# Kernel tuning notes

Hardware: AMD Instinct MI355X
Metric: run time of the kernel (lower is better)

## Reference

```python
import jax, jax.numpy as jnp
import numpy as np

EPS = 1e-8  # torch CosineSimilarity default eps


def setup_inputs() -> dict:
    key = jax.random.key(0)
    k1, k2, k3, k4, k5, k6, k7, k8 = jax.random.split(key, 8)
    N1, N2 = 8192, 8192
    # first 3 cols: geometric features; col 3: integer class label stored as float
    e1_feat = jax.random.normal(k1, (N1, 3), dtype=jnp.float32)
    e2_feat = jax.random.normal(k2, (N2, 3), dtype=jnp.float32)
    e1_cls = jax.random.randint(k3, (N1, 1), 0, 8).astype(jnp.float32)
    e2_cls = jax.random.randint(k4, (N2, 1), 0, 8).astype(jnp.float32)
    edges1 = jnp.concatenate([e1_feat, e1_cls], axis=-1)
    edges2 = jnp.concatenate([e2_feat, e2_cls], axis=-1)
    W1 = jax.random.normal(k5, (3, 64), dtype=jnp.float32) * 0.5
    b1 = jax.random.normal(k6, (64,), dtype=jnp.float32) * 0.1
    W2 = jax.random.normal(k7, (64, 32), dtype=jnp.float32) * 0.1
    b2 = jax.random.normal(k8, (32,), dtype=jnp.float32) * 0.1
    return {"edges1": edges1, "edges2": edges2, "W1": W1, "b1": b1, "W2": W2, "b2": b2}


def _branch(x, W1, b1, W2, b2):
    h = jax.nn.relu(x @ W1 + b1)
    return h @ W2 + b2  # [N, 32]


def reference(edges1, edges2, W1, b1, W2, b2):
    f1 = _branch(edges1[:, :3], W1, b1, W2, b2)  # [N1, 32]
    f2 = _branch(edges2[:, :3], W1, b1, W2, b2)  # [N2, 32]
    # pairwise cosine similarity without materializing [N1, N2, 32]
    dots = jnp.einsum('id,jd->ij', f1, f2)                  # [N1, N2]
    n1 = jnp.linalg.norm(f1, axis=-1)                        # [N1]
    n2 = jnp.linalg.norm(f2, axis=-1)                        # [N2]
    denom = jnp.maximum(n1[:, None] * n2[None, :], EPS)
    dist_mat = dots / denom                                  # [N1, N2]
    # pairwise label-equality mask (all label columns must match)
    cls1 = edges1[:, 3:].astype(jnp.int32)                   # [N1, C]
    cls2 = edges2[:, 3:].astype(jnp.int32)                   # [N2, C]
    cls_aff = jnp.all(cls1[:, None, :] == cls2[None, :, :], axis=-1)  # [N1, N2] bool
    return cls_aff.astype(dist_mat.dtype) * dist_mat
```

## Files before the change

kernel.cpp:

```cpp
#include <hip/hip_runtime.h>


typedef __bf16 bf16x8 __attribute__((ext_vector_type(8)));
typedef float floatx4 __attribute__((ext_vector_type(4)));

__global__ __launch_bounds__(256) void mlp_norm_kernel(
    const float* __restrict__ e1, const float* __restrict__ e2,
    const float* __restrict__ W1, const float* __restrict__ b1,
    const float* __restrict__ W2, const float* __restrict__ b2,
    __bf16* __restrict__ f1b, __bf16* __restrict__ f2b,
    int* __restrict__ cls1, int* __restrict__ cls2, int N1, int N2)
{
    __shared__ float sW1[192];
    __shared__ float sb1[64];
    __shared__ float sW2[2048];
    __shared__ float sb2[32];
    for (int i = threadIdx.x; i < 192; i += 256) sW1[i] = W1[i];
    if (threadIdx.x < 64) sb1[threadIdx.x] = b1[threadIdx.x];
    for (int i = threadIdx.x; i < 2048; i += 256) sW2[i] = W2[i];
    if (threadIdx.x < 32) sb2[threadIdx.x] = b2[threadIdx.x];
    __syncthreads();

    int t = blockIdx.x * 256 + threadIdx.x;
    if (t >= N1 + N2) return;

    const float* src;
    __bf16* fout;
    int* cout;
    int row;
    if (t < N1) { row = t;      src = e1 + (size_t)row * 4; fout = f1b; cout = cls1; }
    else        { row = t - N1; src = e2 + (size_t)row * 4; fout = f2b; cout = cls2; }

    float x0 = src[0], x1 = src[1], x2 = src[2];
    int lbl = (int)src[3];

    float f[32];
#pragma unroll
    for (int k = 0; k < 32; ++k) f[k] = sb2[k];

    for (int j = 0; j < 64; ++j) {
        float h = fmaf(x0, sW1[j], fmaf(x1, sW1[64 + j], fmaf(x2, sW1[128 + j], sb1[j])));
        h = fmaxf(h, 0.0f);
#pragma unroll
        for (int k = 0; k < 32; ++k) f[k] = fmaf(h, sW2[j * 32 + k], f[k]);
    }

    float ss = 0.0f;
#pragma unroll
    for (int k = 0; k < 32; ++k) ss = fmaf(f[k], f[k], ss);
    float n = sqrtf(ss);
    float scale = (n > 1e-20f) ? (1.0f / n) : 0.0f;

    __bf16* dst = fout + (size_t)row * 32;
#pragma unroll
    for (int k = 0; k < 32; ++k) dst[k] = (__bf16)(f[k] * scale);
    cout[row] = lbl;
}

__global__ __launch_bounds__(256) void pair_cos_kernel(
    const __bf16* __restrict__ f1b, const __bf16* __restrict__ f2b,
    const int* __restrict__ cls1, const int* __restrict__ cls2,
    float* __restrict__ out, int N2, int ncg)
{
    const int lane = threadIdx.x & 63;
    const int wid = blockIdx.x * 4 + (threadIdx.x >> 6);
    const int istrip = wid / ncg;
    const int cg = wid - istrip * ncg;
    const int i0 = istrip * 16;
    const int j0 = cg * 512;
    const int r16 = lane & 15;
    const int q = lane >> 4;

    bf16x8 a = *(const bf16x8*)(f1b + (size_t)(i0 + r16) * 32 + q * 8);
    int4 c1 = *(const int4*)(cls1 + i0 + q * 4);

    const size_t row_base = (size_t)(i0 + q * 4) * N2;

#pragma unroll 4
    for (int tIdx = 0; tIdx < 32; ++tIdx) {
        int j = j0 + tIdx * 16;
        bf16x8 b = *(const bf16x8*)(f2b + (size_t)(j + r16) * 32 + q * 8);
        int c2 = cls2[j + r16];

        floatx4 acc = {0.0f, 0.0f, 0.0f, 0.0f};
        floatx4 d = __builtin_amdgcn_mfma_f32_16x16x32_bf16(a, b, acc, 0, 0, 0);

        float* outp = out + row_base + j + r16;
        outp[0]            = (c1.x == c2) ? d[0] : 0.0f;
        outp[(size_t)N2]   = (c1.y == c2) ? d[1] : 0.0f;
        outp[(size_t)N2*2] = (c1.z == c2) ? d[2] : 0.0f;
        outp[(size_t)N2*3] = (c1.w == c2) ? d[3] : 0.0f;
    }
}

extern "C" void kernel_launch(void* const* d_in, const int* in_sizes, int n_in,
                              void* d_out, int out_size, void* d_ws, size_t ws_size,
                              hipStream_t stream) {
    const float* e1 = (const float*)d_in[0];
    const float* e2 = (const float*)d_in[1];
    const float* W1 = (const float*)d_in[2];
    const float* b1 = (const float*)d_in[3];
    const float* W2 = (const float*)d_in[4];
    const float* b2 = (const float*)d_in[5];
    float* out = (float*)d_out;

    const int N1 = in_sizes[0] / 4;
    const int N2 = in_sizes[1] / 4;

    char* ws = (char*)d_ws;
    __bf16* f1b = (__bf16*)ws;
    __bf16* f2b = (__bf16*)(ws + (size_t)N1 * 64);
    int* cls1 = (int*)(ws + (size_t)(N1 + N2) * 64);
    int* cls2 = cls1 + N1;

    int nrows = N1 + N2;
    mlp_norm_kernel<<<(nrows + 255) / 256, 256, 0, stream>>>(
        e1, e2, W1, b1, W2, b2, f1b, f2b, cls1, cls2, N1, N2);

    int ncg = N2 / 512;
    int nwaves = (N1 / 16) * ncg;
    pair_cos_kernel<<<nwaves / 4, 256, 0, stream>>>(
        f1b, f2b, cls1, cls2, out, N2, ncg);
}
```

Before: 276.0 us.

## Stage cosine tiles in LDS for coalesced 16-byte nontemporal output stores

The pair kernel now gives each block a 16x512 output tile. It swaps the MFMA operands so each lane holds four consecutive columns, writes the masked results into a padded shared-memory tile, then streams whole rows to global memory with 16-byte nontemporal stores. Before, each lane issued scattered 4-byte stores across four rows. The MLP kernel moves to 64-thread blocks with vectorized float4 reads of W2 from LDS and a partially unrolled hidden loop. The costs are about 33KB of LDS per block, which may limit occupancy, and an extra block-wide barrier.

```diff
diff --git a/kernel.cpp b/kernel.cpp
--- a/kernel.cpp
+++ b/kernel.cpp
@@ -4,24 +4,24 @@
 typedef __bf16 bf16x8 __attribute__((ext_vector_type(8)));
 typedef float floatx4 __attribute__((ext_vector_type(4)));
 
-__global__ __launch_bounds__(256) void mlp_norm_kernel(
+__global__ __launch_bounds__(64) void mlp_norm_kernel(
     const float* __restrict__ e1, const float* __restrict__ e2,
     const float* __restrict__ W1, const float* __restrict__ b1,
     const float* __restrict__ W2, const float* __restrict__ b2,
     __bf16* __restrict__ f1b, __bf16* __restrict__ f2b,
     int* __restrict__ cls1, int* __restrict__ cls2, int N1, int N2)
 {
-    __shared__ float sW1[192];
+    __shared__ __align__(16) float sW1[192];
     __shared__ float sb1[64];
-    __shared__ float sW2[2048];
+    __shared__ __align__(16) float sW2[2048];
     __shared__ float sb2[32];
-    for (int i = threadIdx.x; i < 192; i += 256) sW1[i] = W1[i];
-    if (threadIdx.x < 64) sb1[threadIdx.x] = b1[threadIdx.x];
-    for (int i = threadIdx.x; i < 2048; i += 256) sW2[i] = W2[i];
+    for (int i = threadIdx.x; i < 192; i += 64) sW1[i] = W1[i];
+    sb1[threadIdx.x] = b1[threadIdx.x];
+    for (int i = threadIdx.x; i < 2048; i += 64) sW2[i] = W2[i];
     if (threadIdx.x < 32) sb2[threadIdx.x] = b2[threadIdx.x];
     __syncthreads();
 
-    int t = blockIdx.x * 256 + threadIdx.x;
+    int t = blockIdx.x * 64 + threadIdx.x;
     if (t >= N1 + N2) return;
 
     const float* src;
@@ -38,11 +38,19 @@
 #pragma unroll
     for (int k = 0; k < 32; ++k) f[k] = sb2[k];
 
+#pragma unroll 4
     for (int j = 0; j < 64; ++j) {
         float h = fmaf(x0, sW1[j], fmaf(x1, sW1[64 + j], fmaf(x2, sW1[128 + j], sb1[j])));
         h = fmaxf(h, 0.0f);
+        const floatx4* w2 = (const floatx4*)(sW2 + j * 32);
 #pragma unroll
-        for (int k = 0; k < 32; ++k) f[k] = fmaf(h, sW2[j * 32 + k], f[k]);
+        for (int k4 = 0; k4 < 8; ++k4) {
+            floatx4 w = w2[k4];
+            f[k4 * 4 + 0] = fmaf(h, w[0], f[k4 * 4 + 0]);
+            f[k4 * 4 + 1] = fmaf(h, w[1], f[k4 * 4 + 1]);
+            f[k4 * 4 + 2] = fmaf(h, w[2], f[k4 * 4 + 2]);
+            f[k4 * 4 + 3] = fmaf(h, w[3], f[k4 * 4 + 3]);
+        }
     }
 
     float ss = 0.0f;
@@ -57,39 +65,54 @@
     cout[row] = lbl;
 }
 
+#define TROW 520
 __global__ __launch_bounds__(256) void pair_cos_kernel(
     const __bf16* __restrict__ f1b, const __bf16* __restrict__ f2b,
     const int* __restrict__ cls1, const int* __restrict__ cls2,
     float* __restrict__ out, int N2, int ncg)
 {
+    __shared__ __align__(16) float tile[16 * TROW];
+
     const int lane = threadIdx.x & 63;
-    const int wid = blockIdx.x * 4 + (threadIdx.x >> 6);
-    const int istrip = wid / ncg;
-    const int cg = wid - istrip * ncg;
+    const int w = threadIdx.x >> 6;
+    const int istrip = blockIdx.x / ncg;
+    const int cg = blockIdx.x - istrip * ncg;
     const int i0 = istrip * 16;
     const int j0 = cg * 512;
     const int r16 = lane & 15;
     const int q = lane >> 4;
 
-    bf16x8 a = *(const bf16x8*)(f1b + (size_t)(i0 + r16) * 32 + q * 8);
-    int4 c1 = *(const int4*)(cls1 + i0 + q * 4);
+    bf16x8 bfrag = *(const bf16x8*)(f1b + (size_t)(i0 + r16) * 32 + q * 8);
+    const int c1 = cls1[i0 + r16];
 
-    const size_t row_base = (size_t)(i0 + q * 4) * N2;
-
-#pragma unroll 4
-    for (int tIdx = 0; tIdx < 32; ++tIdx) {
-        int j = j0 + tIdx * 16;
-        bf16x8 b = *(const bf16x8*)(f2b + (size_t)(j + r16) * 32 + q * 8);
-        int c2 = cls2[j + r16];
+#pragma unroll
+    for (int t = 0; t < 8; ++t) {
+        const int jc = w * 128 + t * 16;
+        const int j = j0 + jc;
+        bf16x8 afrag = *(const bf16x8*)(f2b + (size_t)(j + r16) * 32 + q * 8);
+        int4 c2 = *(const int4*)(cls2 + j + q * 4);
 
         floatx4 acc = {0.0f, 0.0f, 0.0f, 0.0f};
-        floatx4 d = __builtin_amdgcn_mfma_f32_16x16x32_bf16(a, b, acc, 0, 0, 0);
+        floatx4 d = __builtin_amdgcn_mfma_f32_16x16x32_bf16(afrag, bfrag, acc, 0, 0, 0);
 
-        float* outp = out + row_base + j + r16;
-        outp[0]            = (c1.x == c2) ? d[0] : 0.0f;
-        outp[(size_t)N2]   = (c1.y == c2) ? d[1] : 0.0f;
-        outp[(size_t)N2*2] = (c1.z == c2) ? d[2] : 0.0f;
-        outp[(size_t)N2*3] = (c1.w == c2) ? d[3] : 0.0f;
+        floatx4 m;
+        m[0] = (c2.x == c1) ? d[0] : 0.0f;
+        m[1] = (c2.y == c1) ? d[1] : 0.0f;
+        m[2] = (c2.z == c1) ? d[2] : 0.0f;
+        m[3] = (c2.w == c1) ? d[3] : 0.0f;
+        *(floatx4*)(tile + r16 * TROW + jc + q * 4) = m;
+    }
+
+    __syncthreads();
+
+    const int r = threadIdx.x >> 7;
+    const int cb = (threadIdx.x & 127) << 2;
+    const size_t obase = (size_t)i0 * N2 + j0 + cb;
+#pragma unroll
+    for (int rr0 = 0; rr0 < 16; rr0 += 2) {
+        const int rr = rr0 + r;
+        floatx4 v = *(const floatx4*)(tile + rr * TROW + cb);
+        __builtin_nontemporal_store(v, (floatx4*)(out + obase + (size_t)rr * N2));
     }
 }
 
@@ -114,11 +137,11 @@
     int* cls2 = cls1 + N1;
 
     int nrows = N1 + N2;
-    mlp_norm_kernel<<<(nrows + 255) / 256, 256, 0, stream>>>(
+    mlp_norm_kernel<<<(nrows + 63) / 64, 64, 0, stream>>>(
         e1, e2, W1, b1, W2, b2, f1b, f2b, cls1, cls2, N1, N2);
 
     int ncg = N2 / 512;
-    int nwaves = (N1 / 16) * ncg;
-    pair_cos_kernel<<<nwaves / 4, 256, 0, stream>>>(
+    int nblocks = (N1 / 16) * ncg;
+    pair_cos_kernel<<<nblocks, 256, 0, stream>>>(
         f1b, f2b, cls1, cls2, out, N2, ncg);
 }
```

After: 287.3 us. 1.04x slower.
